# Optimization experiments

Hardware: AMD Instinct MI355X
Metric: run time of the kernel (lower is better)

## Reference

```python
import jax, jax.numpy as jnp
import numpy as np

DIM = 64  # module-level global `dim` used as the softmax scale


def setup_inputs() -> dict:
    key = jax.random.key(0)
    kq, kk, kv, km = jax.random.split(key, 4)
    B, H, S, d = 4, 16, 2048, DIM
    Q = jax.random.normal(kq, (B, H, S, d), dtype=jnp.float32)
    K = jax.random.normal(kk, (B, H, S, d), dtype=jnp.float32)
    V = jax.random.normal(kv, (B, H, S, d), dtype=jnp.float32)
    attn_mask = jax.random.randint(km, (B, H, S, S), 0, 2).astype(jnp.bool_)
    return {"Q": Q, "K": K, "V": V, "attn_mask": attn_mask}


def reference(Q, K, V, attn_mask):
    scale = 1.0 / np.sqrt(DIM).astype(np.float32)
    # scores: [B, H, S, S]
    scores = jnp.einsum("bhqd,bhkd->bhqk", Q, K) * scale
    # NOTE: original torch code does masked_fill_(attn_mask, 0) — fills with 0, not -inf
    scores = jnp.where(attn_mask, jnp.zeros((), scores.dtype), scores)
    attn = jax.nn.softmax(scores, axis=-1)
    context = jnp.einsum("bhqk,bhkd->bhqd", attn, V)
    return context
```

## Files before the change

kernel.cpp:

```cpp
#include <hip/hip_runtime.h>
#include <hip/hip_bf16.h>

typedef __bf16 bf16;
typedef __attribute__((ext_vector_type(8))) __bf16 bf16x8;
typedef __attribute__((ext_vector_type(4))) __bf16 bf16x4;
typedef __attribute__((ext_vector_type(4))) float f32x4;
typedef __attribute__((ext_vector_type(4))) int i32x4;

constexpr int SLEN = 2048;
constexpr int DH = 64;
constexpr int NBH = 64;
constexpr float SCALE_LOG2E = 0.125f * 1.4426950408889634f;

__global__ void cast_k_kernel(const float* __restrict__ in, bf16* __restrict__ out) {
    size_t i = (size_t)blockIdx.x * blockDim.x + threadIdx.x;
    const float4* p = (const float4*)in + i * 2;
    float4 a = p[0], b = p[1];
    bf16x8 v;
    v[0]=(bf16)a.x; v[1]=(bf16)a.y; v[2]=(bf16)a.z; v[3]=(bf16)a.w;
    v[4]=(bf16)b.x; v[5]=(bf16)b.y; v[6]=(bf16)b.z; v[7]=(bf16)b.w;
    ((bf16x8*)out)[i] = v;
}

__global__ void transpose_v_kernel(const float* __restrict__ V, bf16* __restrict__ Vt) {
    __shared__ float t[64][65];
    int bh = blockIdx.y;
    int s0 = blockIdx.x * 64;
    int tx = threadIdx.x & 63, ty = threadIdx.x >> 6;
    const float* vp = V + ((size_t)bh * SLEN + s0) * DH;
    #pragma unroll
    for (int r = ty; r < 64; r += 4) t[r][tx] = vp[(size_t)r * DH + tx];
    __syncthreads();
    bf16* op = Vt + (size_t)bh * DH * SLEN + s0;
    #pragma unroll
    for (int r = ty; r < 64; r += 4) op[(size_t)r * SLEN + tx] = (bf16)t[tx][r];
}

__device__ __forceinline__ void gl_lds16(const void* g, void* l) {
    __builtin_amdgcn_global_load_lds(
        (const __attribute__((address_space(1))) void*)g,
        (__attribute__((address_space(3))) void*)l, 16, 0, 0);
}

__global__ __launch_bounds__(256, 4) void attn_kernel(
    const float* __restrict__ Q, const int* __restrict__ mask,
    const bf16* __restrict__ Kb, const bf16* __restrict__ Vtb,
    float* __restrict__ out)
{
    __shared__ char KT[2][8192];
    __shared__ char VT[2][8192];
    __shared__ char PT[8192];

    const int bh = blockIdx.y;
    const int qbase = blockIdx.x * 64;
    const int tid = threadIdx.x;
    const int w = tid >> 6, l = tid & 63;
    const int lq = l & 15, lg = l >> 4;

    const char* kgb = (const char*)(Kb + (size_t)bh * SLEN * DH);
    const char* vgb = (const char*)(Vtb + (size_t)bh * DH * SLEN);

    const int kv_r = l >> 3;
    const int kv_c = ((l & 7) * 16) ^ (kv_r << 4);

    bf16x8 aq[2];
    {
        const float* qp = Q + ((size_t)bh * SLEN + qbase + w * 16 + lq) * DH + lg * 8;
        #pragma unroll
        for (int t = 0; t < 2; ++t) {
            float4 x = *(const float4*)(qp + t * 32);
            float4 y = *(const float4*)(qp + t * 32 + 4);
            bf16x8 f;
            f[0]=(bf16)x.x; f[1]=(bf16)x.y; f[2]=(bf16)x.z; f[3]=(bf16)x.w;
            f[4]=(bf16)y.x; f[5]=(bf16)y.y; f[6]=(bf16)y.z; f[7]=(bf16)y.w;
            aq[t] = f;
        }
    }

    f32x4 acc[4] = {{0,0,0,0},{0,0,0,0},{0,0,0,0},{0,0,0,0}};
    float dpart = 0.f;
    const int swzk = (lq & 7) << 4;
    const int prow = w * 16 + lq;
    char* pb = PT + prow * 128;
    const int pswz = (prow & 7) << 4;

    auto stage = [&](int kb, int buf) {
        #pragma unroll
        for (int q = 0; q < 2; ++q) {
            int r = (w * 2 + q) * 8 + kv_r;
            gl_lds16(kgb + (size_t)(kb + r) * 128 + kv_c, &KT[buf][(w * 2 + q) * 1024]);
            gl_lds16(vgb + (size_t)r * 4096 + (size_t)kb * 2 + kv_c, &VT[buf][(w * 2 + q) * 1024]);
        }
    };

    const int* mrow = mask + ((size_t)bh * SLEN + qbase + w * 16 + lq) * SLEN;
    i32x4 mcur[4], mnext[4];
    #pragma unroll
    for (int n = 0; n < 4; ++n)
        mcur[n] = __builtin_nontemporal_load((const i32x4*)(mrow + n * 16 + lg * 4));

    stage(0, 0);
    __syncthreads();

    int cur = 0;
    for (int kt = 0; kt < SLEN / 64; ++kt) {
        const bool has_next = (kt + 1) < (SLEN / 64);
        if (has_next) {
            stage((kt + 1) * 64, cur ^ 1);
            #pragma unroll
            for (int n = 0; n < 4; ++n)
                mnext[n] = __builtin_nontemporal_load(
                    (const i32x4*)(mrow + (kt + 1) * 64 + n * 16 + lg * 4));
        }

        #pragma unroll
        for (int n = 0; n < 4; ++n) {
            f32x4 s = {0, 0, 0, 0};
            #pragma unroll
            for (int t = 0; t < 2; ++t) {
                bf16x8 bk = *(const bf16x8*)&KT[cur][(n * 16 + lq) * 128 + ((t * 64 + lg * 16) ^ swzk)];
                s = __builtin_amdgcn_mfma_f32_16x16x32_bf16(bk, aq[t], s, 0, 0, 0);
            }
            bf16x4 pk;
            #pragma unroll
            for (int i = 0; i < 4; ++i) {
                float e = mcur[n][i] ? 0.0f : s[i] * SCALE_LOG2E;
                float p = exp2f(e);
                dpart += p;
                pk[i] = (bf16)p;
            }
            *(bf16x4*)(pb + ((n * 32 + lg * 8) ^ pswz)) = pk;
        }

        #pragma unroll
        for (int n = 0; n < 4; ++n) {
            #pragma unroll
            for (int kk = 0; kk < 2; ++kk) {
                bf16x8 ap = *(const bf16x8*)(pb + ((kk * 64 + lg * 16) ^ pswz));
                bf16x8 bv = *(const bf16x8*)&VT[cur][(n * 16 + lq) * 128 + ((kk * 64 + lg * 16) ^ swzk)];
                acc[n] = __builtin_amdgcn_mfma_f32_16x16x32_bf16(ap, bv, acc[n], 0, 0, 0);
            }
        }

        if (has_next) {
            #pragma unroll
            for (int n = 0; n < 4; ++n) mcur[n] = mnext[n];
        }
        __syncthreads();
        cur ^= 1;
    }

    dpart += __shfl_xor(dpart, 16, 64);
    dpart += __shfl_xor(dpart, 32, 64);
    float dinv = 1.0f / dpart;

    float di[4];
    #pragma unroll
    for (int i = 0; i < 4; ++i) di[i] = __shfl(dinv, lg * 4 + i, 64);

    float* op = out + ((size_t)bh * SLEN + qbase + w * 16) * DH;
    #pragma unroll
    for (int n = 0; n < 4; ++n) {
        #pragma unroll
        for (int i = 0; i < 4; ++i)
            op[(size_t)(lg * 4 + i) * DH + n * 16 + lq] = acc[n][i] * di[i];
    }
}

extern "C" void kernel_launch(void* const* d_in, const int* in_sizes, int n_in,
                              void* d_out, int out_size, void* d_ws, size_t ws_size,
                              hipStream_t stream) {
    const float* Q    = (const float*)d_in[0];
    const float* K    = (const float*)d_in[1];
    const float* V    = (const float*)d_in[2];
    const int*   mask = (const int*)d_in[3];
    float* out = (float*)d_out;

    bf16* Kb  = (bf16*)d_ws;
    bf16* Vtb = Kb + (size_t)NBH * SLEN * DH;

    int n8 = NBH * SLEN * DH / 8;
    cast_k_kernel<<<n8 / 256, 256, 0, stream>>>(K, Kb);
    transpose_v_kernel<<<dim3(SLEN / 64, NBH), 256, 0, stream>>>(V, Vtb);
    attn_kernel<<<dim3(SLEN / 64, NBH), 256, 0, stream>>>(Q, mask, Kb, Vtb, out);
}
```

Baseline: 323.2 us.

## Fuse K/V prep kernels, remap blocks per XCD, unroll pipeline with finer waits

```diff
diff --git a/kernel.cpp b/kernel.cpp
--- a/kernel.cpp
+++ b/kernel.cpp
@@ -12,24 +12,34 @@
 constexpr int NBH = 64;
 constexpr float SCALE_LOG2E = 0.125f * 1.4426950408889634f;
 
-__global__ void cast_k_kernel(const float* __restrict__ in, bf16* __restrict__ out) {
-    size_t i = (size_t)blockIdx.x * blockDim.x + threadIdx.x;
-    const float4* p = (const float4*)in + i * 2;
-    float4 a = p[0], b = p[1];
-    bf16x8 v;
-    v[0]=(bf16)a.x; v[1]=(bf16)a.y; v[2]=(bf16)a.z; v[3]=(bf16)a.w;
-    v[4]=(bf16)b.x; v[5]=(bf16)b.y; v[6]=(bf16)b.z; v[7]=(bf16)b.w;
-    ((bf16x8*)out)[i] = v;
-}
-
-__global__ void transpose_v_kernel(const float* __restrict__ V, bf16* __restrict__ Vt) {
+__global__ __launch_bounds__(256) void prep_kv_kernel(
+    const float* __restrict__ K, const float* __restrict__ V,
+    bf16* __restrict__ Kb, bf16* __restrict__ Vt)
+{
     __shared__ float t[64][65];
-    int bh = blockIdx.y;
-    int s0 = blockIdx.x * 64;
-    int tx = threadIdx.x & 63, ty = threadIdx.x >> 6;
+    const int bh = blockIdx.y;
+    const int s0 = blockIdx.x * 64;
+    const int tx = threadIdx.x & 63, ty = threadIdx.x >> 6;
+
     const float* vp = V + ((size_t)bh * SLEN + s0) * DH;
     #pragma unroll
     for (int r = ty; r < 64; r += 4) t[r][tx] = vp[(size_t)r * DH + tx];
+
+    {
+        const float* kp = K + ((size_t)bh * SLEN + s0) * DH;
+        bf16* kbp = Kb + ((size_t)bh * SLEN + s0) * DH;
+        int r = threadIdx.x >> 2, c = (threadIdx.x & 3) * 16;
+        const float4* src = (const float4*)(kp + (size_t)r * DH + c);
+        float4 a = src[0], b = src[1], c2 = src[2], d = src[3];
+        bf16x8 o0, o1;
+        o0[0]=(bf16)a.x;  o0[1]=(bf16)a.y;  o0[2]=(bf16)a.z;  o0[3]=(bf16)a.w;
+        o0[4]=(bf16)b.x;  o0[5]=(bf16)b.y;  o0[6]=(bf16)b.z;  o0[7]=(bf16)b.w;
+        o1[0]=(bf16)c2.x; o1[1]=(bf16)c2.y; o1[2]=(bf16)c2.z; o1[3]=(bf16)c2.w;
+        o1[4]=(bf16)d.x;  o1[5]=(bf16)d.y;  o1[6]=(bf16)d.z;  o1[7]=(bf16)d.w;
+        *(bf16x8*)(kbp + (size_t)r * DH + c)     = o0;
+        *(bf16x8*)(kbp + (size_t)r * DH + c + 8) = o1;
+    }
+
     __syncthreads();
     bf16* op = Vt + (size_t)bh * DH * SLEN + s0;
     #pragma unroll
@@ -51,8 +61,10 @@
     __shared__ char VT[2][8192];
     __shared__ char PT[8192];
 
-    const int bh = blockIdx.y;
-    const int qbase = blockIdx.x * 64;
+    const int h = blockIdx.x;
+    const int logical = (h & 7) * 256 + (h >> 3);
+    const int bh = logical >> 5;
+    const int qbase = (logical & 31) * 64;
     const int tid = threadIdx.x;
     const int w = tid >> 6, l = tid & 63;
     const int lq = l & 15, lg = l >> 4;
@@ -84,7 +96,10 @@
     char* pb = PT + prow * 128;
     const int pswz = (prow & 7) << 4;
 
-    auto stage = [&](int kb, int buf) {
+    const int* mrow = mask + ((size_t)bh * SLEN + qbase + w * 16 + lq) * SLEN;
+
+    auto stage = [&](int t, int buf) {
+        const int kb = t * 64;
         #pragma unroll
         for (int q = 0; q < 2; ++q) {
             int r = (w * 2 + q) * 8 + kv_r;
@@ -92,27 +107,12 @@
             gl_lds16(vgb + (size_t)r * 4096 + (size_t)kb * 2 + kv_c, &VT[buf][(w * 2 + q) * 1024]);
         }
     };
-
-    const int* mrow = mask + ((size_t)bh * SLEN + qbase + w * 16 + lq) * SLEN;
-    i32x4 mcur[4], mnext[4];
-    #pragma unroll
-    for (int n = 0; n < 4; ++n)
-        mcur[n] = __builtin_nontemporal_load((const i32x4*)(mrow + n * 16 + lg * 4));
-
-    stage(0, 0);
-    __syncthreads();
-
-    int cur = 0;
-    for (int kt = 0; kt < SLEN / 64; ++kt) {
-        const bool has_next = (kt + 1) < (SLEN / 64);
-        if (has_next) {
-            stage((kt + 1) * 64, cur ^ 1);
-            #pragma unroll
-            for (int n = 0; n < 4; ++n)
-                mnext[n] = __builtin_nontemporal_load(
-                    (const i32x4*)(mrow + (kt + 1) * 64 + n * 16 + lg * 4));
-        }
-
+    auto loadmask = [&](int t, i32x4* m) {
+        #pragma unroll
+        for (int n = 0; n < 4; ++n)
+            m[n] = __builtin_nontemporal_load((const i32x4*)(mrow + t * 64 + n * 16 + lg * 4));
+    };
+    auto body = [&](int cur, const i32x4* mC) {
         #pragma unroll
         for (int n = 0; n < 4; ++n) {
             f32x4 s = {0, 0, 0, 0};
@@ -124,14 +124,13 @@
             bf16x4 pk;
             #pragma unroll
             for (int i = 0; i < 4; ++i) {
-                float e = mcur[n][i] ? 0.0f : s[i] * SCALE_LOG2E;
+                float e = mC[n][i] ? 0.0f : s[i] * SCALE_LOG2E;
                 float p = exp2f(e);
                 dpart += p;
                 pk[i] = (bf16)p;
             }
             *(bf16x4*)(pb + ((n * 32 + lg * 8) ^ pswz)) = pk;
         }
-
         #pragma unroll
         for (int n = 0; n < 4; ++n) {
             #pragma unroll
@@ -141,13 +140,35 @@
                 acc[n] = __builtin_amdgcn_mfma_f32_16x16x32_bf16(ap, bv, acc[n], 0, 0, 0);
             }
         }
-
-        if (has_next) {
-            #pragma unroll
-            for (int n = 0; n < 4; ++n) mcur[n] = mnext[n];
-        }
-        __syncthreads();
-        cur ^= 1;
+    };
+    auto tile_sync = [&]() {
+        asm volatile("s_waitcnt vmcnt(4) lgkmcnt(0)" ::: "memory");
+        __builtin_amdgcn_s_barrier();
+        __builtin_amdgcn_sched_barrier(0);
+    };
+
+    i32x4 mA[4], mB[4];
+
+    stage(0, 0);
+    __builtin_amdgcn_sched_barrier(0);
+    loadmask(0, mA);
+    tile_sync();
+
+    for (int kt = 0; kt < SLEN / 64; kt += 2) {
+        stage(kt + 1, 1);
+        __builtin_amdgcn_sched_barrier(0);
+        loadmask(kt + 1, mB);
+        body(0, mA);
+        tile_sync();
+
+        const bool more = (kt + 2) < (SLEN / 64);
+        if (more) {
+            stage(kt + 2, 0);
+            __builtin_amdgcn_sched_barrier(0);
+            loadmask(kt + 2, mA);
+        }
+        body(1, mB);
+        if (more) tile_sync();
     }
 
     dpart += __shfl_xor(dpart, 16, 64);
@@ -179,8 +200,6 @@
     bf16* Kb  = (bf16*)d_ws;
     bf16* Vtb = Kb + (size_t)NBH * SLEN * DH;
 
-    int n8 = NBH * SLEN * DH / 8;
-    cast_k_kernel<<<n8 / 256, 256, 0, stream>>>(K, Kb);
-    transpose_v_kernel<<<dim3(SLEN / 64, NBH), 256, 0, stream>>>(V, Vtb);
-    attn_kernel<<<dim3(SLEN / 64, NBH), 256, 0, stream>>>(Q, mask, Kb, Vtb, out);
-}
+    prep_kv_kernel<<<dim3(SLEN / 64, NBH), 256, 0, stream>>>(K, V, Kb, Vtb);
+    attn_kernel<<<2048, 256, 0, stream>>>(Q, mask, Kb, Vtb, out);
+}
```

Measured after the change: 312.3 us. 1.03x faster.
